# Performance work log

Measured on AMD Instinct MI355X. Metric: run time of the kernel, lower is better.

The kernel has to match this reference:

```python
import jax, jax.numpy as jnp
import numpy as np

N_NODES = 10000
N_EDGES = 640000
N_GRAPHS = 64
D = 128
N_BLOCKS = 2
NEG_SLOPE = 0.01  # F.leaky_relu default


def setup_inputs() -> dict:
    key = jax.random.key(0)
    ks = jax.random.split(key, 9)
    x = jax.random.normal(ks[0], (N_NODES, D), dtype=jnp.float32)
    edge_src = jax.random.randint(ks[1], (N_EDGES,), 0, N_NODES, dtype=jnp.int32)
    edge_dst = jax.random.randint(ks[2], (N_EDGES,), 0, N_NODES, dtype=jnp.int32)
    graph_ids = jnp.sort(jax.random.randint(ks[3], (N_NODES,), 0, N_GRAPHS, dtype=jnp.int32))
    s = 1.414 / np.sqrt(D)  # xavier-normal-ish scale
    Wfc = jax.random.normal(ks[4], (N_BLOCKS, D, D), dtype=jnp.float32) * s
    bfc = jnp.zeros((N_BLOCKS, D), dtype=jnp.float32)
    wl = jax.random.normal(ks[5], (N_BLOCKS, D), dtype=jnp.float32) * s
    wr = jax.random.normal(ks[6], (N_BLOCKS, D), dtype=jnp.float32) * s
    Wres = jax.random.normal(ks[7], (N_BLOCKS, D, D), dtype=jnp.float32) * s
    return {"x": x, "edge_src": edge_src, "edge_dst": edge_dst, "graph_ids": graph_ids,
            "Wfc": Wfc, "bfc": bfc, "wl": wl, "wr": wr, "Wres": Wres}


def _gat_block(x, edge_src, edge_dst, Wfc_b, bfc_b, wl_b, wr_b, Wres_b):
    # node projections: nn.Linear -> x @ W^T + b
    feat = x @ Wfc_b.T + bfc_b                       # [N, D]
    a_self = feat @ wl_b                              # [N] self_a (dst side)
    a_nb = feat @ wr_b                                # [N] attn  (src side)
    # per-edge score: leaky_relu(self_a[dst] + attn[src])
    s = a_self[edge_dst] + a_nb[edge_src]             # [E]
    s = jnp.where(s >= 0, s, NEG_SLOPE * s)
    # segment softmax over incoming edges of each dst node
    m = jax.ops.segment_max(s, edge_dst, num_segments=N_NODES)   # [N]
    e = jnp.exp(s - m[edge_dst])                                  # [E]
    denom = jax.ops.segment_sum(e, edge_dst, num_segments=N_NODES)
    w = e / denom[edge_dst]                                       # [E]
    # attention-weighted neighbor aggregation
    accum = jax.ops.segment_sum(w[:, None] * feat[edge_src], edge_dst,
                                num_segments=N_NODES)             # [N, D]
    # residual (in_size == out_size -> res_fc, no bias), then relu
    out = accum + x @ Wres_b.T
    return jax.nn.relu(out)


def reference(x, edge_src, edge_dst, graph_ids, Wfc, bfc, wl, wr, Wres):
    blocks = [
        _gat_block(x, edge_src, edge_dst, Wfc[b], bfc[b], wl[b], wr[b], Wres[b])
        for b in range(N_BLOCKS)
    ]
    h = jnp.concatenate(blocks, axis=1)               # mode='concat' -> [N, 2*D]
    # dgl.sum_nodes: per-graph sum pooling
    phis = jax.ops.segment_sum(h, graph_ids, num_segments=N_GRAPHS)  # [G, 2*D]
    return h, phis
```

## Files before the change

kernel.cpp:

```cpp
#include <hip/hip_runtime.h>
#include <hip/hip_bf16.h>
#include <math.h>

#define N_NODES 10000
#define N_EDGES 640000
#define N_GRAPHS 64
#define DIM 128
#define NEG_SLOPE 0.01f
#define NB_CSR 128
#define EDGES_PER_BLK (N_EDGES / NB_CSR)


__global__ __launch_bounds__(512) void csr_hist(const int4* __restrict__ edst4,
                                                int* __restrict__ bh) {
    __shared__ int hist[N_NODES];
    const int blk = blockIdx.x;
    const int t = threadIdx.x;
    for (int n = t; n < N_NODES; n += 512) hist[n] = 0;
    __syncthreads();
    const int base4 = blk * (EDGES_PER_BLK / 4);
    for (int i = t; i < EDGES_PER_BLK / 4; i += 512) {
        int4 d = edst4[base4 + i];
        atomicAdd(&hist[d.x], 1);
        atomicAdd(&hist[d.y], 1);
        atomicAdd(&hist[d.z], 1);
        atomicAdd(&hist[d.w], 1);
    }
    __syncthreads();
    int* dst = bh + (size_t)blk * N_NODES;
    for (int n = t; n < N_NODES; n += 512) dst[n] = hist[n];
}

__global__ __launch_bounds__(256) void csr_node_scan(int* __restrict__ bh,
                                                     int* __restrict__ deg) {
    int n = blockIdx.x * 256 + threadIdx.x;
    if (n >= N_NODES) return;
    int running = 0;
    for (int blk = 0; blk < NB_CSR; ++blk) {
        int* p = bh + (size_t)blk * N_NODES + n;
        int v = *p;
        *p = running;
        running += v;
    }
    deg[n] = running;
}

__global__ __launch_bounds__(1024) void scan_deg(const int* __restrict__ deg,
                                                 int* __restrict__ rowptr) {
    __shared__ int sdata[1024];
    const int tid = threadIdx.x;
    const int base = tid * 10;
    int cnt = N_NODES - base;
    if (cnt < 0) cnt = 0;
    if (cnt > 10) cnt = 10;
    int local[10];
    int s = 0;
    for (int i = 0; i < cnt; ++i) { local[i] = s; s += deg[base + i]; }
    sdata[tid] = s;
    __syncthreads();
    for (int off = 1; off < 1024; off <<= 1) {
        int v = 0;
        if (tid >= off) v = sdata[tid - off];
        __syncthreads();
        if (tid >= off) sdata[tid] += v;
        __syncthreads();
    }
    int pre = (tid == 0) ? 0 : sdata[tid - 1];
    for (int i = 0; i < cnt; ++i) rowptr[base + i] = pre + local[i];
    if (tid == 1023) rowptr[N_NODES] = sdata[1023];
}

__global__ __launch_bounds__(512) void csr_scatter(
    const int4* __restrict__ esrc4, const int4* __restrict__ edst4,
    const int* __restrict__ rowptr, const int* __restrict__ bh,
    int* __restrict__ csr_src) {
    __shared__ int cur[N_NODES];
    const int blk = blockIdx.x;
    const int t = threadIdx.x;
    const int* boff = bh + (size_t)blk * N_NODES;
    for (int n = t; n < N_NODES; n += 512) cur[n] = rowptr[n] + boff[n];
    __syncthreads();
    const int base4 = blk * (EDGES_PER_BLK / 4);
    for (int i = t; i < EDGES_PER_BLK / 4; i += 512) {
        int4 s = esrc4[base4 + i];
        int4 d = edst4[base4 + i];
        csr_src[atomicAdd(&cur[d.x], 1)] = s.x;
        csr_src[atomicAdd(&cur[d.y], 1)] = s.y;
        csr_src[atomicAdd(&cur[d.z], 1)] = s.z;
        csr_src[atomicAdd(&cur[d.w], 1)] = s.w;
    }
}

__device__ __forceinline__ unsigned short f2bf(float f) {
    __hip_bfloat16 h = __float2bfloat16(f);
    return *reinterpret_cast<unsigned short*>(&h);
}

__global__ __launch_bounds__(256) void gemm_xwT(
    const float* __restrict__ x, const float* __restrict__ Wfc,
    const float* __restrict__ bfc, const float* __restrict__ Wres,
    float* __restrict__ feat, float* __restrict__ resid,
    unsigned short* __restrict__ feat_b16,
    const float* __restrict__ wl, const float* __restrict__ wr,
    float* __restrict__ a_self, float* __restrict__ a_nb) {
    const int which = blockIdx.z & 1;
    const int b = blockIdx.z >> 1;
    const float* __restrict__ W = (which ? Wres : Wfc) + b * DIM * DIM;
    float* __restrict__ out = (which ? resid : feat) + (size_t)b * N_NODES * DIM;
    const int n0 = blockIdx.x * 64;
    const int j0 = blockIdx.y * 64;

    __shared__ float xs[32][68];
    __shared__ float wsh[32][68];

    const int t = threadIdx.x;
    const int tj = t & 15;
    const int tn = t >> 4;
    const int r = t >> 2;
    const int q = t & 3;

    float acc[4][4];
#pragma unroll
    for (int i = 0; i < 4; ++i)
#pragma unroll
        for (int j = 0; j < 4; ++j) acc[i][j] = 0.f;

    for (int kc = 0; kc < DIM; kc += 32) {
        {
            float v[8];
            int n = n0 + r;
            if (n < N_NODES) {
                const float* p = x + (size_t)n * DIM + kc + q * 8;
                float4 v0 = *reinterpret_cast<const float4*>(p);
                float4 v1 = *reinterpret_cast<const float4*>(p + 4);
                v[0] = v0.x; v[1] = v0.y; v[2] = v0.z; v[3] = v0.w;
                v[4] = v1.x; v[5] = v1.y; v[6] = v1.z; v[7] = v1.w;
            } else {
#pragma unroll
                for (int m = 0; m < 8; ++m) v[m] = 0.f;
            }
#pragma unroll
            for (int m = 0; m < 8; ++m) xs[q * 8 + m][r] = v[m];

            const float* pw = W + (size_t)(j0 + r) * DIM + kc + q * 8;
            float4 w0 = *reinterpret_cast<const float4*>(pw);
            float4 w1 = *reinterpret_cast<const float4*>(pw + 4);
            float wv[8] = {w0.x, w0.y, w0.z, w0.w, w1.x, w1.y, w1.z, w1.w};
#pragma unroll
            for (int m = 0; m < 8; ++m) wsh[q * 8 + m][r] = wv[m];
        }
        __syncthreads();

#pragma unroll
        for (int k = 0; k < 32; ++k) {
            float4 xv = *reinterpret_cast<const float4*>(&xs[k][4 * tn]);
            float4 wv = *reinterpret_cast<const float4*>(&wsh[k][4 * tj]);
            float xa[4] = {xv.x, xv.y, xv.z, xv.w};
            float wa[4] = {wv.x, wv.y, wv.z, wv.w};
#pragma unroll
            for (int i = 0; i < 4; ++i)
#pragma unroll
                for (int j = 0; j < 4; ++j) acc[i][j] += xa[i] * wa[j];
        }
        __syncthreads();
    }

    float wlv[4], wrv[4];
    if (!which) {
#pragma unroll
        for (int k = 0; k < 4; ++k) {
            wlv[k] = wl[b * DIM + j0 + tj * 4 + k];
            wrv[k] = wr[b * DIM + j0 + tj * 4 + k];
        }
    }

#pragma unroll
    for (int i = 0; i < 4; ++i) {
        int n = n0 + tn * 4 + i;
        int j = j0 + tj * 4;
        float4 o;
        o.x = acc[i][0]; o.y = acc[i][1]; o.z = acc[i][2]; o.w = acc[i][3];
        if (!which) {
            const float* bias = bfc + b * DIM + j;
            o.x += bias[0]; o.y += bias[1]; o.z += bias[2]; o.w += bias[3];
        }
        if (n < N_NODES) {
            *reinterpret_cast<float4*>(out + (size_t)n * DIM + j) = o;
            if (!which) {
                ushort4 u;
                u.x = f2bf(o.x); u.y = f2bf(o.y); u.z = f2bf(o.z); u.w = f2bf(o.w);
                *reinterpret_cast<ushort4*>(
                    feat_b16 + ((size_t)b * N_NODES + n) * DIM + j) = u;
            }
        }
        if (!which) {
            float ps = o.x * wlv[0] + o.y * wlv[1] + o.z * wlv[2] + o.w * wlv[3];
            float pr = o.x * wrv[0] + o.y * wrv[1] + o.z * wrv[2] + o.w * wrv[3];
#pragma unroll
            for (int off = 8; off > 0; off >>= 1) {
                ps += __shfl_xor(ps, off, 64);
                pr += __shfl_xor(pr, off, 64);
            }
            if (tj == 0 && n < N_NODES) {
                atomicAdd(&a_self[b * N_NODES + n], ps);
                atomicAdd(&a_nb[b * N_NODES + n], pr);
            }
        }
    }
}

__global__ __launch_bounds__(256) void aggregate(
    const unsigned short* __restrict__ feat_b16, const float* __restrict__ resid,
    const float* __restrict__ a_self, const float* __restrict__ a_nb,
    const int* __restrict__ rowptr, const int* __restrict__ csr_src,
    float* __restrict__ out) {
    const int wave = threadIdx.x >> 6;
    const int lane = threadIdx.x & 63;
    const int n = blockIdx.x * 4 + wave;
    const int b = blockIdx.y;
    const int q = lane >> 4;
    const int l16 = lane & 15;
    const int start = rowptr[n];
    const int end = rowptr[n + 1];

    const float* __restrict__ anb = a_nb + b * N_NODES;
    const uint4* __restrict__ fb =
        reinterpret_cast<const uint4*>(feat_b16 + (size_t)b * N_NODES * DIM);
    const float asl = a_self[b * N_NODES + n];

    float acc[8];
#pragma unroll
    for (int k = 0; k < 8; ++k) acc[k] = 0.f;
    float dpart = 0.f;

    for (int c = start; c < end; c += 64) {
        int j = c + lane;
        float e = 0.f;
        int src = 0;
        if (j < end) {
            src = csr_src[j];
            float s = asl + anb[src];
            s = (s >= 0.f) ? s : NEG_SLOPE * s;
            e = __expf(s);
        }
        dpart += e;
        int cnt = end - c;
        if (cnt > 64) cnt = 64;
        int iters = (cnt + 3) >> 2;

        float w0 = __shfl(e, q, 64);
        int s0 = __shfl(src, q, 64);
        uint4 f0 = fb[(size_t)s0 * 16 + l16];

        for (int i2 = 0; i2 < iters - 1; ++i2) {
            int idx = (i2 + 1) * 4 + q;
            float w1 = __shfl(e, idx, 64);
            int s1 = __shfl(src, idx, 64);
            uint4 f1 = fb[(size_t)s1 * 16 + l16];
#pragma unroll
            for (int k = 0; k < 4; ++k) {
                unsigned int u = (&f0.x)[k];
                float lo = __uint_as_float(u << 16);
                float hi = __uint_as_float(u & 0xffff0000u);
                acc[2 * k]     += w0 * lo;
                acc[2 * k + 1] += w0 * hi;
            }
            w0 = w1; f0 = f1;
        }
#pragma unroll
        for (int k = 0; k < 4; ++k) {
            unsigned int u = (&f0.x)[k];
            float lo = __uint_as_float(u << 16);
            float hi = __uint_as_float(u & 0xffff0000u);
            acc[2 * k]     += w0 * lo;
            acc[2 * k + 1] += w0 * hi;
        }
    }

#pragma unroll
    for (int k = 0; k < 8; ++k) {
        acc[k] += __shfl_xor(acc[k], 16, 64);
        acc[k] += __shfl_xor(acc[k], 32, 64);
    }
    float denom = dpart;
#pragma unroll
    for (int off = 32; off > 0; off >>= 1) denom += __shfl_xor(denom, off, 64);

    if (q == 0) {
        float inv = (end > start) ? 1.f / denom : 0.f;
        const float4* rr = reinterpret_cast<const float4*>(
            resid + ((size_t)b * N_NODES + n) * DIM);
        float4 r0 = rr[l16 * 2];
        float4 r1 = rr[l16 * 2 + 1];
        float4 o0, o1;
        o0.x = fmaxf(acc[0] * inv + r0.x, 0.f);
        o0.y = fmaxf(acc[1] * inv + r0.y, 0.f);
        o0.z = fmaxf(acc[2] * inv + r0.z, 0.f);
        o0.w = fmaxf(acc[3] * inv + r0.w, 0.f);
        o1.x = fmaxf(acc[4] * inv + r1.x, 0.f);
        o1.y = fmaxf(acc[5] * inv + r1.y, 0.f);
        o1.z = fmaxf(acc[6] * inv + r1.z, 0.f);
        o1.w = fmaxf(acc[7] * inv + r1.w, 0.f);
        float4* po = reinterpret_cast<float4*>(out + (size_t)n * (2 * DIM) + b * DIM);
        po[l16 * 2] = o0;
        po[l16 * 2 + 1] = o1;
    }
}

__device__ int lower_bound_dev(const int* __restrict__ a, int n, int key) {
    int lo = 0, hi = n;
    while (lo < hi) {
        int mid = (lo + hi) >> 1;
        if (a[mid] < key) lo = mid + 1;
        else hi = mid;
    }
    return lo;
}

__global__ __launch_bounds__(256) void pool_graphs(
    const float* __restrict__ h, const int* __restrict__ gids,
    float* __restrict__ phis) {
    const int g = blockIdx.x;
    const int chunk = blockIdx.y;
    const int tid = threadIdx.x;
    int lo = lower_bound_dev(gids, N_NODES, g);
    int hi = lower_bound_dev(gids, N_NODES, g + 1);
    float acc = 0.f;
    for (int n = lo + chunk; n < hi; n += 16) acc += h[(size_t)n * (2 * DIM) + tid];
    if (acc != 0.f) atomicAdd(&phis[(size_t)g * (2 * DIM) + tid], acc);
}

extern "C" void kernel_launch(void* const* d_in, const int* in_sizes, int n_in,
                              void* d_out, int out_size, void* d_ws, size_t ws_size,
                              hipStream_t stream) {
    const float* x    = (const float*)d_in[0];
    const int* esrc   = (const int*)d_in[1];
    const int* edst   = (const int*)d_in[2];
    const int* gids   = (const int*)d_in[3];
    const float* Wfc  = (const float*)d_in[4];
    const float* bfc  = (const float*)d_in[5];
    const float* wl   = (const float*)d_in[6];
    const float* wr   = (const float*)d_in[7];
    const float* Wres = (const float*)d_in[8];
    float* out = (float*)d_out;

    char* ws = (char*)d_ws;
    float* feat    = (float*)(ws + 0);
    float* resid   = (float*)(ws + 10240000);
    float* a_self  = (float*)(ws + 20480000);
    float* a_nb    = (float*)(ws + 20560000);
    int*   deg     = (int*)(ws + 20640000);
    int*   rowptr  = (int*)(ws + 20688000);
    int*   csr_src = (int*)(ws + 20784000);
    unsigned short* feat_b16 = (unsigned short*)(ws + 23344000);
    int*   bh      = (int*)(ws + 28464000);

    float* phis = out + (size_t)N_NODES * 2 * DIM;

    hipMemsetAsync(a_self, 0, 4 * N_NODES * sizeof(float), stream);
    hipMemsetAsync(phis, 0, N_GRAPHS * 2 * DIM * sizeof(float), stream);

    csr_hist<<<NB_CSR, 512, 0, stream>>>((const int4*)edst, bh);
    csr_node_scan<<<(N_NODES + 255) / 256, 256, 0, stream>>>(bh, deg);
    scan_deg<<<1, 1024, 0, stream>>>(deg, rowptr);
    csr_scatter<<<NB_CSR, 512, 0, stream>>>(
        (const int4*)esrc, (const int4*)edst, rowptr, bh, csr_src);

    gemm_xwT<<<dim3((N_NODES + 63) / 64, 2, 4), 256, 0, stream>>>(
        x, Wfc, bfc, Wres, feat, resid, feat_b16, wl, wr, a_self, a_nb);
    aggregate<<<dim3(2500, 2), 256, 0, stream>>>(
        feat_b16, resid, a_self, a_nb, rowptr, csr_src, out);
    pool_graphs<<<dim3(N_GRAPHS, 16), 256, 0, stream>>>(out, gids, phis);
}
```

Before: 167.5 us.

## Switch projection GEMM to bf16 MFMA and drop memsets and fp32 feat buffer

Replaces the fp32 SIMT tiled projection GEMM with a bf16 MFMA 16x16x32 kernel. Each block now covers all 128 output columns, so the attention dot products are written directly instead of accumulated with atomics. The unused fp32 feat output and both memsets are removed, with the phis zeroing folded into scan_deg. The CSR build kernels move to 1024-thread blocks, and the node scan is vectorised to int4. Rounding x and the weights to bf16 adds precision loss to the residual and the feature projection.

```diff
diff --git a/kernel.cpp b/kernel.cpp
--- a/kernel.cpp
+++ b/kernel.cpp
@@ -10,16 +10,24 @@
 #define NB_CSR 128
 #define EDGES_PER_BLK (N_EDGES / NB_CSR)
 
-
-__global__ __launch_bounds__(512) void csr_hist(const int4* __restrict__ edst4,
-                                                int* __restrict__ bh) {
+typedef __attribute__((ext_vector_type(8))) short bf16x8;
+typedef __attribute__((ext_vector_type(4))) float f32x4;
+
+
+__device__ __forceinline__ unsigned short f2bf(float f) {
+    __hip_bfloat16 h = __float2bfloat16(f);
+    return *reinterpret_cast<unsigned short*>(&h);
+}
+
+__global__ __launch_bounds__(1024) void csr_hist(const int4* __restrict__ edst4,
+                                                 int* __restrict__ bh) {
     __shared__ int hist[N_NODES];
     const int blk = blockIdx.x;
     const int t = threadIdx.x;
-    for (int n = t; n < N_NODES; n += 512) hist[n] = 0;
+    for (int n = t; n < N_NODES; n += 1024) hist[n] = 0;
     __syncthreads();
     const int base4 = blk * (EDGES_PER_BLK / 4);
-    for (int i = t; i < EDGES_PER_BLK / 4; i += 512) {
+    for (int i = t; i < EDGES_PER_BLK / 4; i += 1024) {
         int4 d = edst4[base4 + i];
         atomicAdd(&hist[d.x], 1);
         atomicAdd(&hist[d.y], 1);
@@ -28,27 +36,30 @@
     }
     __syncthreads();
     int* dst = bh + (size_t)blk * N_NODES;
-    for (int n = t; n < N_NODES; n += 512) dst[n] = hist[n];
+    for (int n = t; n < N_NODES; n += 1024) dst[n] = hist[n];
 }
 
 __global__ __launch_bounds__(256) void csr_node_scan(int* __restrict__ bh,
                                                      int* __restrict__ deg) {
-    int n = blockIdx.x * 256 + threadIdx.x;
-    if (n >= N_NODES) return;
-    int running = 0;
+    int n4 = blockIdx.x * 256 + threadIdx.x;
+    if (n4 >= N_NODES / 4) return;
+    int4 run = {0, 0, 0, 0};
     for (int blk = 0; blk < NB_CSR; ++blk) {
-        int* p = bh + (size_t)blk * N_NODES + n;
-        int v = *p;
-        *p = running;
-        running += v;
-    }
-    deg[n] = running;
+        int4* p = reinterpret_cast<int4*>(bh + (size_t)blk * N_NODES) + n4;
+        int4 v = *p;
+        *p = run;
+        run.x += v.x; run.y += v.y; run.z += v.z; run.w += v.w;
+    }
+    reinterpret_cast<int4*>(deg)[n4] = run;
 }
 
 __global__ __launch_bounds__(1024) void scan_deg(const int* __restrict__ deg,
-                                                 int* __restrict__ rowptr) {
+                                                 int* __restrict__ rowptr,
+                                                 float* __restrict__ phis) {
     __shared__ int sdata[1024];
     const int tid = threadIdx.x;
+    for (int i = tid; i < N_GRAPHS * 2 * DIM; i += 1024) phis[i] = 0.f;
+
     const int base = tid * 10;
     int cnt = N_NODES - base;
     if (cnt < 0) cnt = 0;
@@ -70,7 +81,7 @@
     if (tid == 1023) rowptr[N_NODES] = sdata[1023];
 }
 
-__global__ __launch_bounds__(512) void csr_scatter(
+__global__ __launch_bounds__(1024) void csr_scatter(
     const int4* __restrict__ esrc4, const int4* __restrict__ edst4,
     const int* __restrict__ rowptr, const int* __restrict__ bh,
     int* __restrict__ csr_src) {
@@ -78,10 +89,10 @@
     const int blk = blockIdx.x;
     const int t = threadIdx.x;
     const int* boff = bh + (size_t)blk * N_NODES;
-    for (int n = t; n < N_NODES; n += 512) cur[n] = rowptr[n] + boff[n];
+    for (int n = t; n < N_NODES; n += 1024) cur[n] = rowptr[n] + boff[n];
     __syncthreads();
     const int base4 = blk * (EDGES_PER_BLK / 4);
-    for (int i = t; i < EDGES_PER_BLK / 4; i += 512) {
+    for (int i = t; i < EDGES_PER_BLK / 4; i += 1024) {
         int4 s = esrc4[base4 + i];
         int4 d = edst4[base4 + i];
         csr_src[atomicAdd(&cur[d.x], 1)] = s.x;
@@ -91,120 +102,137 @@
     }
 }
 
-__device__ __forceinline__ unsigned short f2bf(float f) {
-    __hip_bfloat16 h = __float2bfloat16(f);
-    return *reinterpret_cast<unsigned short*>(&h);
-}
-
-__global__ __launch_bounds__(256) void gemm_xwT(
+__global__ __launch_bounds__(256) void gemm_mfma(
     const float* __restrict__ x, const float* __restrict__ Wfc,
     const float* __restrict__ bfc, const float* __restrict__ Wres,
-    float* __restrict__ feat, float* __restrict__ resid,
-    unsigned short* __restrict__ feat_b16,
     const float* __restrict__ wl, const float* __restrict__ wr,
+    float* __restrict__ resid, unsigned short* __restrict__ feat_b16,
     float* __restrict__ a_self, float* __restrict__ a_nb) {
-    const int which = blockIdx.z & 1;
-    const int b = blockIdx.z >> 1;
+    const int which = blockIdx.y & 1;
+    const int b = blockIdx.y >> 1;
     const float* __restrict__ W = (which ? Wres : Wfc) + b * DIM * DIM;
-    float* __restrict__ out = (which ? resid : feat) + (size_t)b * N_NODES * DIM;
     const int n0 = blockIdx.x * 64;
-    const int j0 = blockIdx.y * 64;
-
-    __shared__ float xs[32][68];
-    __shared__ float wsh[32][68];
-
     const int t = threadIdx.x;
-    const int tj = t & 15;
-    const int tn = t >> 4;
-    const int r = t >> 2;
-    const int q = t & 3;
-
-    float acc[4][4];
-#pragma unroll
-    for (int i = 0; i < 4; ++i)
-#pragma unroll
-        for (int j = 0; j < 4; ++j) acc[i][j] = 0.f;
-
-    for (int kc = 0; kc < DIM; kc += 32) {
-        {
-            float v[8];
-            int n = n0 + r;
-            if (n < N_NODES) {
-                const float* p = x + (size_t)n * DIM + kc + q * 8;
-                float4 v0 = *reinterpret_cast<const float4*>(p);
-                float4 v1 = *reinterpret_cast<const float4*>(p + 4);
-                v[0] = v0.x; v[1] = v0.y; v[2] = v0.z; v[3] = v0.w;
-                v[4] = v1.x; v[5] = v1.y; v[6] = v1.z; v[7] = v1.w;
-            } else {
-#pragma unroll
-                for (int m = 0; m < 8; ++m) v[m] = 0.f;
+
+    __shared__ unsigned short xs[64][136];
+    __shared__ unsigned short wsh[128][136];
+
+    {
+        const int r = t >> 2, qq = t & 3;
+        const int n = n0 + r;
+        ushort4* drow = reinterpret_cast<ushort4*>(&xs[r][qq * 32]);
+        if (n < N_NODES) {
+            const float4* p = reinterpret_cast<const float4*>(x + (size_t)n * DIM + qq * 32);
+#pragma unroll
+            for (int i = 0; i < 8; ++i) {
+                float4 v = p[i];
+                ushort4 u;
+                u.x = f2bf(v.x); u.y = f2bf(v.y); u.z = f2bf(v.z); u.w = f2bf(v.w);
+                drow[i] = u;
             }
-#pragma unroll
-            for (int m = 0; m < 8; ++m) xs[q * 8 + m][r] = v[m];
-
-            const float* pw = W + (size_t)(j0 + r) * DIM + kc + q * 8;
-            float4 w0 = *reinterpret_cast<const float4*>(pw);
-            float4 w1 = *reinterpret_cast<const float4*>(pw + 4);
-            float wv[8] = {w0.x, w0.y, w0.z, w0.w, w1.x, w1.y, w1.z, w1.w};
-#pragma unroll
-            for (int m = 0; m < 8; ++m) wsh[q * 8 + m][r] = wv[m];
-        }
+        } else {
+            ushort4 z = {0, 0, 0, 0};
+#pragma unroll
+            for (int i = 0; i < 8; ++i) drow[i] = z;
+        }
+    }
+    {
+        const int rw = t >> 1, hh = t & 1;
+        const float4* p = reinterpret_cast<const float4*>(W + (size_t)rw * DIM + hh * 64);
+        ushort4* drow = reinterpret_cast<ushort4*>(&wsh[rw][hh * 64]);
+#pragma unroll
+        for (int i = 0; i < 16; ++i) {
+            float4 v = p[i];
+            ushort4 u;
+            u.x = f2bf(v.x); u.y = f2bf(v.y); u.z = f2bf(v.z); u.w = f2bf(v.w);
+            drow[i] = u;
+        }
+    }
+    __syncthreads();
+
+    const int wave = t >> 6, lane = t & 63;
+    const int quad = lane >> 4, jc = lane & 15;
+    const int m0 = wave * 16;
+
+    bf16x8 af[4];
+#pragma unroll
+    for (int ks = 0; ks < 4; ++ks)
+        af[ks] = *reinterpret_cast<const bf16x8*>(&xs[m0 + jc][ks * 32 + quad * 8]);
+
+    f32x4 accs[8];
+    float ps[4] = {0.f, 0.f, 0.f, 0.f}, pr[4] = {0.f, 0.f, 0.f, 0.f};
+#pragma unroll
+    for (int jt = 0; jt < 8; ++jt) {
+        f32x4 acc = {0.f, 0.f, 0.f, 0.f};
+#pragma unroll
+        for (int ks = 0; ks < 4; ++ks) {
+            bf16x8 bfr = *reinterpret_cast<const bf16x8*>(
+                &wsh[jt * 16 + jc][ks * 32 + quad * 8]);
+            acc = __builtin_amdgcn_mfma_f32_16x16x32_bf16(af[ks], bfr, acc, 0, 0, 0);
+        }
+        if (!which) {
+            float bias = bfc[b * DIM + jt * 16 + jc];
+            acc[0] += bias; acc[1] += bias; acc[2] += bias; acc[3] += bias;
+            float wlv = wl[b * DIM + jt * 16 + jc];
+            float wrv = wr[b * DIM + jt * 16 + jc];
+#pragma unroll
+            for (int r2 = 0; r2 < 4; ++r2) { ps[r2] += acc[r2] * wlv; pr[r2] += acc[r2] * wrv; }
+        }
+        accs[jt] = acc;
+    }
+
+    __syncthreads();
+
+    if (!which) {
+#pragma unroll
+        for (int off = 8; off > 0; off >>= 1) {
+#pragma unroll
+            for (int r2 = 0; r2 < 4; ++r2) {
+                ps[r2] += __shfl_xor(ps[r2], off, 64);
+                pr[r2] += __shfl_xor(pr[r2], off, 64);
+            }
+        }
+        if (jc == 0) {
+#pragma unroll
+            for (int r2 = 0; r2 < 4; ++r2) {
+                int n = n0 + m0 + quad * 4 + r2;
+                if (n < N_NODES) {
+                    a_self[b * N_NODES + n] = ps[r2];
+                    a_nb[b * N_NODES + n] = pr[r2];
+                }
+            }
+        }
+#pragma unroll
+        for (int jt = 0; jt < 8; ++jt)
+#pragma unroll
+            for (int r2 = 0; r2 < 4; ++r2)
+                xs[m0 + quad * 4 + r2][jt * 16 + jc] = f2bf(accs[jt][r2]);
         __syncthreads();
-
-#pragma unroll
-        for (int k = 0; k < 32; ++k) {
-            float4 xv = *reinterpret_cast<const float4*>(&xs[k][4 * tn]);
-            float4 wv = *reinterpret_cast<const float4*>(&wsh[k][4 * tj]);
-            float xa[4] = {xv.x, xv.y, xv.z, xv.w};
-            float wa[4] = {wv.x, wv.y, wv.z, wv.w};
-#pragma unroll
-            for (int i = 0; i < 4; ++i)
-#pragma unroll
-                for (int j = 0; j < 4; ++j) acc[i][j] += xa[i] * wa[j];
-        }
+        const int r = t >> 2, qq = t & 3;
+        const int n = n0 + r;
+        if (n < N_NODES) {
+            uint4* dst = reinterpret_cast<uint4*>(
+                feat_b16 + ((size_t)b * N_NODES + n) * DIM + qq * 32);
+            const uint4* srcp = reinterpret_cast<const uint4*>(&xs[r][qq * 32]);
+#pragma unroll
+            for (int i = 0; i < 4; ++i) dst[i] = srcp[i];
+        }
+    } else {
+        float* fs = reinterpret_cast<float*>(wsh);
+#pragma unroll
+        for (int jt = 0; jt < 8; ++jt)
+#pragma unroll
+            for (int r2 = 0; r2 < 4; ++r2)
+                fs[(m0 + quad * 4 + r2) * 136 + jt * 16 + jc] = accs[jt][r2];
         __syncthreads();
-    }
-
-    float wlv[4], wrv[4];
-    if (!which) {
-#pragma unroll
-        for (int k = 0; k < 4; ++k) {
-            wlv[k] = wl[b * DIM + j0 + tj * 4 + k];
-            wrv[k] = wr[b * DIM + j0 + tj * 4 + k];
-        }
-    }
-
-#pragma unroll
-    for (int i = 0; i < 4; ++i) {
-        int n = n0 + tn * 4 + i;
-        int j = j0 + tj * 4;
-        float4 o;
-        o.x = acc[i][0]; o.y = acc[i][1]; o.z = acc[i][2]; o.w = acc[i][3];
-        if (!which) {
-            const float* bias = bfc + b * DIM + j;
-            o.x += bias[0]; o.y += bias[1]; o.z += bias[2]; o.w += bias[3];
-        }
+        const int r = t >> 2, qq = t & 3;
+        const int n = n0 + r;
         if (n < N_NODES) {
-            *reinterpret_cast<float4*>(out + (size_t)n * DIM + j) = o;
-            if (!which) {
-                ushort4 u;
-                u.x = f2bf(o.x); u.y = f2bf(o.y); u.z = f2bf(o.z); u.w = f2bf(o.w);
-                *reinterpret_cast<ushort4*>(
-                    feat_b16 + ((size_t)b * N_NODES + n) * DIM + j) = u;
-            }
-        }
-        if (!which) {
-            float ps = o.x * wlv[0] + o.y * wlv[1] + o.z * wlv[2] + o.w * wlv[3];
-            float pr = o.x * wrv[0] + o.y * wrv[1] + o.z * wrv[2] + o.w * wrv[3];
-#pragma unroll
-            for (int off = 8; off > 0; off >>= 1) {
-                ps += __shfl_xor(ps, off, 64);
-                pr += __shfl_xor(pr, off, 64);
-            }
-            if (tj == 0 && n < N_NODES) {
-                atomicAdd(&a_self[b * N_NODES + n], ps);
-                atomicAdd(&a_nb[b * N_NODES + n], pr);
-            }
+            float4* dst = reinterpret_cast<float4*>(
+                resid + ((size_t)b * N_NODES + n) * DIM + qq * 32);
+            const float4* srcp = reinterpret_cast<const float4*>(&fs[r * 136 + qq * 32]);
+#pragma unroll
+            for (int i = 0; i < 8; ++i) dst[i] = srcp[i];
         }
     }
 }
@@ -345,29 +373,25 @@
     float* out = (float*)d_out;
 
     char* ws = (char*)d_ws;
-    float* feat    = (float*)(ws + 0);
-    float* resid   = (float*)(ws + 10240000);
-    float* a_self  = (float*)(ws + 20480000);
-    float* a_nb    = (float*)(ws + 20560000);
-    int*   deg     = (int*)(ws + 20640000);
-    int*   rowptr  = (int*)(ws + 20688000);
-    int*   csr_src = (int*)(ws + 20784000);
-    unsigned short* feat_b16 = (unsigned short*)(ws + 23344000);
-    int*   bh      = (int*)(ws + 28464000);
+    float* resid   = (float*)(ws + 0);
+    float* a_self  = (float*)(ws + 10240000);
+    float* a_nb    = (float*)(ws + 10320000);
+    int*   deg     = (int*)(ws + 10400000);
+    int*   rowptr  = (int*)(ws + 10440000);
+    int*   csr_src = (int*)(ws + 10480032);
+    unsigned short* feat_b16 = (unsigned short*)(ws + 13040032);
+    int*   bh      = (int*)(ws + 18160032);
 
     float* phis = out + (size_t)N_NODES * 2 * DIM;
 
-    hipMemsetAsync(a_self, 0, 4 * N_NODES * sizeof(float), stream);
-    hipMemsetAsync(phis, 0, N_GRAPHS * 2 * DIM * sizeof(float), stream);
-
-    csr_hist<<<NB_CSR, 512, 0, stream>>>((const int4*)edst, bh);
-    csr_node_scan<<<(N_NODES + 255) / 256, 256, 0, stream>>>(bh, deg);
-    scan_deg<<<1, 1024, 0, stream>>>(deg, rowptr);
-    csr_scatter<<<NB_CSR, 512, 0, stream>>>(
+    csr_hist<<<NB_CSR, 1024, 0, stream>>>((const int4*)edst, bh);
+    csr_node_scan<<<(N_NODES / 4 + 255) / 256, 256, 0, stream>>>(bh, deg);
+    scan_deg<<<1, 1024, 0, stream>>>(deg, rowptr, phis);
+    csr_scatter<<<NB_CSR, 1024, 0, stream>>>(
         (const int4*)esrc, (const int4*)edst, rowptr, bh, csr_src);
 
-    gemm_xwT<<<dim3((N_NODES + 63) / 64, 2, 4), 256, 0, stream>>>(
-        x, Wfc, bfc, Wres, feat, resid, feat_b16, wl, wr, a_self, a_nb);
+    gemm_mfma<<<dim3((N_NODES + 63) / 64, 4), 256, 0, stream>>>(
+        x, Wfc, bfc, Wres, wl, wr, resid, feat_b16, a_self, a_nb);
     aggregate<<<dim3(2500, 2), 256, 0, stream>>>(
         feat_b16, resid, a_self, a_nb, rowptr, csr_src, out);
     pool_graphs<<<dim3(N_GRAPHS, 16), 256, 0, stream>>>(out, gids, phis);
```

Result: no change. 169.8 us (+1.3%).
